# Performance work log

Measured on AMD Instinct MI355X. Metric: run time of the kernel, lower is better.

The kernel has to match this reference:

```python
import jax, jax.numpy as jnp
import numpy as np

N_PIX = 196608  # 12 * 128**2 (HEALPix nside=128)
F = 32          # filters (Fin == Fout for residual)
DM = 2          # depth multiplier


def _cheb_sep_conv(x, idx, wnb, wd, wp, b):
    """Separable Chebyshev graph conv.
    x: [B,N,F] maps; idx: [N,nb] neighbor indices; wnb: [N,nb] Laplacian weights;
    wd: [K,F,DM] depthwise Chebyshev weights; wp: [F*DM,Fout] pointwise; b: [Fout].
    """
    def L(t):  # sparse Laplacian apply via fixed-degree neighbor gather
        return jnp.einsum('bnjf,nj->bnf', t[:, idx, :], wnb)
    K = wd.shape[0]
    Ts = [x, L(x)]
    for _ in range(K - 2):  # Chebyshev recursion T_k = 2 L T_{k-1} - T_{k-2}
        Ts.append(2.0 * L(Ts[-1]) - Ts[-2])
    T = jnp.stack(Ts, 0)                      # [K,B,N,F]
    y = jnp.einsum('kbnf,kfd->bnfd', T, wd)   # depthwise over Chebyshev orders
    Bb, Nn, Ff, Dd = y.shape
    y = y.reshape(Bb, Nn, Ff * Dd)
    return y @ wp + b                         # pointwise mix to Fout


def _layernorm(x, gamma, beta, eps=1e-6):
    mu = jnp.mean(x, axis=-1, keepdims=True)
    var = jnp.mean(jnp.square(x - mu), axis=-1, keepdims=True)
    return (x - mu) * jax.lax.rsqrt(var + eps) * gamma + beta


def setup_inputs() -> dict:
    key = jax.random.key(0)
    ks = jax.random.split(key, 10)
    inp = {
        'maps': jax.random.normal(ks[0], (1, N_PIX, F), jnp.float32),
        'idx1': jax.random.randint(ks[1], (N_PIX, 8), 0, N_PIX, jnp.int32),
        'w1_nb': jax.random.normal(ks[2], (N_PIX, 8), jnp.float32) * 0.1,
        'idx2': jax.random.randint(ks[3], (N_PIX, 20), 0, N_PIX, jnp.int32),
        'w2_nb': jax.random.normal(ks[4], (N_PIX, 20), jnp.float32) * 0.1,
        'wd1': jax.random.normal(ks[5], (6, F, DM), jnp.float32) * 0.1,
        'wp1': jax.random.normal(ks[6], (F * DM, F), jnp.float32) * 0.1,
        'b1': jnp.zeros((F,), jnp.float32),
        'gamma1': jnp.ones((F,), jnp.float32),
        'beta1': jnp.zeros((F,), jnp.float32),
        'wd2': jax.random.normal(ks[7], (10, F, DM), jnp.float32) * 0.1,
        'wp2': jax.random.normal(ks[8], (F * DM, F), jnp.float32) * 0.1,
        'b2': jnp.zeros((F,), jnp.float32),
        'gamma2': jnp.ones((F,), jnp.float32),
        'beta2': jnp.zeros((F,), jnp.float32),
    }
    return inp


def reference(maps, idx1, w1_nb, idx2, w2_nb, wd1, wp1, b1, gamma1, beta1,
              wd2, wp2, b2, gamma2, beta2):
    res = maps
    x = _cheb_sep_conv(maps, idx1, w1_nb, wd1, wp1, b1)   # K=6, nb=8
    x = jax.nn.relu(x)
    x = _layernorm(x, gamma1, beta1)
    x = _cheb_sep_conv(x, idx2, w2_nb, wd2, wp2, b2)      # K=10, nb=20
    x = jax.nn.relu(x)
    x = _layernorm(x, gamma2, beta2)
    return x + res
```

## Files before the change

### kernel.cpp

```cpp
#include <hip/hip_runtime.h>

constexpr int NPIX = 196608;
constexpr int FF   = 32;
constexpr size_t SLOT = (size_t)NPIX * FF;

typedef short bf16x8 __attribute__((ext_vector_type(8)));
typedef float f32x4  __attribute__((ext_vector_type(4)));

__device__ __forceinline__ float blo(uint u) {
    union { float f; uint i; } v; v.i = u << 16; return v.f;
}
__device__ __forceinline__ float bhi(uint u) {
    union { float f; uint i; } v; v.i = u & 0xffff0000u; return v.f;
}
__device__ __forceinline__ ushort f2b(float f) {
    union { float f; uint i; } v; v.f = f;
    uint r = v.i + 0x7fffu + ((v.i >> 16) & 1u);
    return (ushort)(r >> 16);
}
__device__ __forceinline__ uint pack2(float lo, float hi) {
    return ((uint)f2b(hi) << 16) | (uint)f2b(lo);
}

__global__ __launch_bounds__(256) void f2b_kernel(const float* __restrict__ src,
                                                  ushort* __restrict__ dst) {
    int i = (blockIdx.x * 256 + threadIdx.x) * 4;
    float4 v = *reinterpret_cast<const float4*>(src + i);
    ushort4 o;
    o.x = f2b(v.x); o.y = f2b(v.y); o.z = f2b(v.z); o.w = f2b(v.w);
    *reinterpret_cast<ushort4*>(dst + i) = o;
}

template<int NB, bool INIT>
__global__ __launch_bounds__(256, 4) void cheb_step4(
    const ushort* __restrict__ Tprev,
    const ushort* __restrict__ Told,
    ushort*       __restrict__ Tout,
    const int*    __restrict__ idx,
    const float*  __restrict__ wnb)
{
    int t = blockIdx.x * 256 + threadIdx.x;
    int n = t >> 2;
    int h = t & 3;

    const int4*   ip = reinterpret_cast<const int4*>(idx + (size_t)n * NB);
    const float4* wv = reinterpret_cast<const float4*>(wnb + (size_t)n * NB);
    int4   I[NB / 4];
    float4 W[NB / 4];
#pragma unroll
    for (int j = 0; j < NB / 4; ++j) { I[j] = ip[j]; W[j] = wv[j]; }

    const uint4* Tp = reinterpret_cast<const uint4*>(Tprev);
    float s0 = 0.f, s1 = 0.f, s2 = 0.f, s3 = 0.f;
    float s4 = 0.f, s5 = 0.f, s6 = 0.f, s7 = 0.f;

#pragma unroll
    for (int j = 0; j < NB / 4; ++j) {
        int4 i4 = I[j]; float4 w4 = W[j];
        {
            uint4 u = Tp[(size_t)i4.x * 4 + h];
            s0 += w4.x * blo(u.x); s1 += w4.x * bhi(u.x);
            s2 += w4.x * blo(u.y); s3 += w4.x * bhi(u.y);
            s4 += w4.x * blo(u.z); s5 += w4.x * bhi(u.z);
            s6 += w4.x * blo(u.w); s7 += w4.x * bhi(u.w);
        }
        {
            uint4 u = Tp[(size_t)i4.y * 4 + h];
            s0 += w4.y * blo(u.x); s1 += w4.y * bhi(u.x);
            s2 += w4.y * blo(u.y); s3 += w4.y * bhi(u.y);
            s4 += w4.y * blo(u.z); s5 += w4.y * bhi(u.z);
            s6 += w4.y * blo(u.w); s7 += w4.y * bhi(u.w);
        }
        {
            uint4 u = Tp[(size_t)i4.z * 4 + h];
            s0 += w4.z * blo(u.x); s1 += w4.z * bhi(u.x);
            s2 += w4.z * blo(u.y); s3 += w4.z * bhi(u.y);
            s4 += w4.z * blo(u.z); s5 += w4.z * bhi(u.z);
            s6 += w4.z * blo(u.w); s7 += w4.z * bhi(u.w);
        }
        {
            uint4 u = Tp[(size_t)i4.w * 4 + h];
            s0 += w4.w * blo(u.x); s1 += w4.w * bhi(u.x);
            s2 += w4.w * blo(u.y); s3 += w4.w * bhi(u.y);
            s4 += w4.w * blo(u.z); s5 += w4.w * bhi(u.z);
            s6 += w4.w * blo(u.w); s7 += w4.w * bhi(u.w);
        }
    }

    size_t base = (size_t)n * 4 + h;
    uint4 o;
    if (INIT) {
        o.x = pack2(s0, s1); o.y = pack2(s2, s3);
        o.z = pack2(s4, s5); o.w = pack2(s6, s7);
    } else {
        uint4 told = reinterpret_cast<const uint4*>(Told)[base];
        o.x = pack2(2.f * s0 - blo(told.x), 2.f * s1 - bhi(told.x));
        o.y = pack2(2.f * s2 - blo(told.y), 2.f * s3 - bhi(told.y));
        o.z = pack2(2.f * s4 - blo(told.z), 2.f * s5 - bhi(told.z));
        o.w = pack2(2.f * s6 - blo(told.w), 2.f * s7 - bhi(told.w));
    }
    reinterpret_cast<uint4*>(Tout)[base] = o;
}

template<int K, bool RESIDUAL, bool OUT_BF16>
__global__ __launch_bounds__(256, 4) void finish_gemm(
    const ushort* __restrict__ chain,
    const float*  __restrict__ wd,
    const float*  __restrict__ wp,
    const float*  __restrict__ bias,
    const float*  __restrict__ gamma,
    const float*  __restrict__ beta,
    const float*  __restrict__ resid,
    void*         __restrict__ outp)
{
    constexpr int KW = K * 32;
    constexpr int WSTRIDE = KW + 8;
    __shared__ float swp[64 * 33];
    __shared__ __align__(16) ushort sW[32][WSTRIDE];

    int tid = threadIdx.x;
    int wv = tid >> 6, l = tid & 63;
    int r = l & 15, hi = l >> 4;
    int nbase = blockIdx.x * 64 + wv * 16;

    bf16x8 aF[K];
#pragma unroll
    for (int k = 0; k < K; ++k)
        aF[k] = *reinterpret_cast<const bf16x8*>(
            chain + (size_t)k * SLOT + (size_t)(nbase + r) * FF + hi * 8);

    for (int i = tid; i < 64 * 32; i += 256) {
        int u = i >> 5, g = i & 31;
        swp[u * 33 + g] = wp[i];
    }
    __syncthreads();

    for (int i = tid; i < 32 * KW; i += 256) {
        int g = i / KW, kf = i - g * KW;
        int f = kf & 31;
        float2 wdv = *reinterpret_cast<const float2*>(wd + (size_t)kf * 2);
        float w2 = wdv.x * swp[(2 * f) * 33 + g] + wdv.y * swp[(2 * f + 1) * 33 + g];
        sW[g][kf] = f2b(w2);
    }
    __syncthreads();

    f32x4 acc0 = {0.f, 0.f, 0.f, 0.f};
    f32x4 acc1 = {0.f, 0.f, 0.f, 0.f};
#pragma unroll
    for (int k = 0; k < K; ++k) {
        bf16x8 b0 = *reinterpret_cast<const bf16x8*>(&sW[r][k * 32 + hi * 8]);
        bf16x8 b1 = *reinterpret_cast<const bf16x8*>(&sW[16 + r][k * 32 + hi * 8]);
        acc0 = __builtin_amdgcn_mfma_f32_16x16x32_bf16(aF[k], b0, acc0, 0, 0, 0);
        acc1 = __builtin_amdgcn_mfma_f32_16x16x32_bf16(aF[k], b1, acc1, 0, 0, 0);
    }

    float bias_lo = bias[r],  bias_hi = bias[16 + r];
    float gam_lo  = gamma[r], gam_hi  = gamma[16 + r];
    float bet_lo  = beta[r],  bet_hi  = beta[16 + r];

#pragma unroll
    for (int v = 0; v < 4; ++v) {
        acc0[v] = fmaxf(acc0[v] + bias_lo, 0.f);
        acc1[v] = fmaxf(acc1[v] + bias_hi, 0.f);
    }
#pragma unroll
    for (int v = 0; v < 4; ++v) {
        float s1 = acc0[v] + acc1[v];
        float s2 = acc0[v] * acc0[v] + acc1[v] * acc1[v];
#pragma unroll
        for (int m = 1; m < 16; m <<= 1) {
            s1 += __shfl_xor(s1, m);
            s2 += __shfl_xor(s2, m);
        }
        float mu  = s1 * (1.f / 32.f);
        float var = s2 * (1.f / 32.f) - mu * mu;
        float rs  = rsqrtf(var + 1e-6f);
        int n = nbase + hi * 4 + v;
        size_t o0 = (size_t)n * FF + r;
        size_t o1 = o0 + 16;
        float z0 = (acc0[v] - mu) * rs * gam_lo + bet_lo;
        float z1 = (acc1[v] - mu) * rs * gam_hi + bet_hi;
        if (RESIDUAL) { z0 += resid[o0]; z1 += resid[o1]; }
        if (OUT_BF16) {
            ((ushort*)outp)[o0] = f2b(z0);
            ((ushort*)outp)[o1] = f2b(z1);
        } else {
            ((float*)outp)[o0] = z0;
            ((float*)outp)[o1] = z1;
        }
    }
}

extern "C" void kernel_launch(void* const* d_in, const int* in_sizes, int n_in,
                              void* d_out, int out_size, void* d_ws, size_t ws_size,
                              hipStream_t stream) {
    const float* maps = (const float*)d_in[0];
    const int*   idx1 = (const int*)  d_in[1];
    const float* w1nb = (const float*)d_in[2];
    const int*   idx2 = (const int*)  d_in[3];
    const float* w2nb = (const float*)d_in[4];
    const float* wd1  = (const float*)d_in[5];
    const float* wp1  = (const float*)d_in[6];
    const float* b1   = (const float*)d_in[7];
    const float* g1   = (const float*)d_in[8];
    const float* be1  = (const float*)d_in[9];
    const float* wd2  = (const float*)d_in[10];
    const float* wp2  = (const float*)d_in[11];
    const float* b2   = (const float*)d_in[12];
    const float* g2   = (const float*)d_in[13];
    const float* be2  = (const float*)d_in[14];
    float* out = (float*)d_out;

    ushort* slots = (ushort*)d_ws;
    ushort* B = slots;
    ushort* A = slots + 4 * SLOT;

    const int stepBlocks = NPIX * 4 / 256;
    const int cvtBlocks  = NPIX * FF / (256 * 4);
    const int finBlocks  = NPIX / 64;

    f2b_kernel<<<cvtBlocks, 256, 0, stream>>>(maps, A);
    cheb_step4<8, true><<<stepBlocks, 256, 0, stream>>>(A, nullptr, A + SLOT, idx1, w1nb);
    cheb_step4<8, false><<<stepBlocks, 256, 0, stream>>>(A + SLOT,     A,              A + 2 * SLOT, idx1, w1nb);
    cheb_step4<8, false><<<stepBlocks, 256, 0, stream>>>(A + 2 * SLOT, A + SLOT,       A + 3 * SLOT, idx1, w1nb);
    cheb_step4<8, false><<<stepBlocks, 256, 0, stream>>>(A + 3 * SLOT, A + 2 * SLOT,   A + 4 * SLOT, idx1, w1nb);
    cheb_step4<8, false><<<stepBlocks, 256, 0, stream>>>(A + 4 * SLOT, A + 3 * SLOT,   A + 5 * SLOT, idx1, w1nb);
    finish_gemm<6, false, true><<<finBlocks, 256, 0, stream>>>(A, wd1, wp1, b1, g1, be1, nullptr, B);

    cheb_step4<20, true><<<stepBlocks, 256, 0, stream>>>(B, nullptr, B + SLOT, idx2, w2nb);
    for (int k = 2; k <= 9; ++k)
        cheb_step4<20, false><<<stepBlocks, 256, 0, stream>>>(
            B + (size_t)(k - 1) * SLOT, B + (size_t)(k - 2) * SLOT,
            B + (size_t)k * SLOT, idx2, w2nb);
    finish_gemm<10, true, false><<<finBlocks, 256, 0, stream>>>(B, wd2, wp2, b2, g2, be2, maps, out);
}
```

Measured before the change: 766.2 us.

## Split feature maps into four planar 8-channel groups for cache-local gathers

After: 1.397 ms. 82.3% more time.

```diff
diff --git a/kernel.cpp b/kernel.cpp
--- a/kernel.cpp
+++ b/kernel.cpp
@@ -6,6 +6,8 @@
 
 typedef short bf16x8 __attribute__((ext_vector_type(8)));
 typedef float f32x4  __attribute__((ext_vector_type(4)));
+typedef int   i32x4  __attribute__((ext_vector_type(4)));
+typedef uint  u32x4  __attribute__((ext_vector_type(4)));
 
 __device__ __forceinline__ float blo(uint u) {
     union { float f; uint i; } v; v.i = u << 16; return v.f;
@@ -22,87 +24,76 @@
     return ((uint)f2b(hi) << 16) | (uint)f2b(lo);
 }
 
-__global__ __launch_bounds__(256) void f2b_kernel(const float* __restrict__ src,
-                                                  ushort* __restrict__ dst) {
-    int i = (blockIdx.x * 256 + threadIdx.x) * 4;
-    float4 v = *reinterpret_cast<const float4*>(src + i);
-    ushort4 o;
-    o.x = f2b(v.x); o.y = f2b(v.y); o.z = f2b(v.z); o.w = f2b(v.w);
-    *reinterpret_cast<ushort4*>(dst + i) = o;
+__global__ __launch_bounds__(256) void regroup_f2b(const float* __restrict__ src,
+                                                   ushort* __restrict__ dst) {
+    int t = blockIdx.x * 256 + threadIdx.x;
+    int n = t >> 2, g = t & 3;
+    const f32x4* sp = reinterpret_cast<const f32x4*>(src + (size_t)n * FF + g * 8);
+    f32x4 a = sp[0], b = sp[1];
+    u32x4 o;
+    o.x = pack2(a.x, a.y); o.y = pack2(a.z, a.w);
+    o.z = pack2(b.x, b.y); o.w = pack2(b.z, b.w);
+    reinterpret_cast<u32x4*>(dst)[(size_t)g * NPIX + n] = o;
 }
 
 template<int NB, bool INIT>
-__global__ __launch_bounds__(256, 4) void cheb_step4(
+__global__ __launch_bounds__(256, 4) void cheb_stepG(
     const ushort* __restrict__ Tprev,
     const ushort* __restrict__ Told,
     ushort*       __restrict__ Tout,
     const int*    __restrict__ idx,
     const float*  __restrict__ wnb)
 {
-    int t = blockIdx.x * 256 + threadIdx.x;
-    int n = t >> 2;
-    int h = t & 3;
-
-    const int4*   ip = reinterpret_cast<const int4*>(idx + (size_t)n * NB);
-    const float4* wv = reinterpret_cast<const float4*>(wnb + (size_t)n * NB);
-    int4   I[NB / 4];
-    float4 W[NB / 4];
-#pragma unroll
-    for (int j = 0; j < NB / 4; ++j) { I[j] = ip[j]; W[j] = wv[j]; }
-
-    const uint4* Tp = reinterpret_cast<const uint4*>(Tprev);
+    int b = blockIdx.x;
+    int g = b & 3;
+    int n = (b >> 2) * 256 + threadIdx.x;
+
+    i32x4 I[NB / 4];
+    f32x4 W[NB / 4];
+    const i32x4* ip = reinterpret_cast<const i32x4*>(idx + (size_t)n * NB);
+    const f32x4* wv = reinterpret_cast<const f32x4*>(wnb + (size_t)n * NB);
+#pragma unroll
+    for (int j = 0; j < NB / 4; ++j) {
+        I[j] = __builtin_nontemporal_load(ip + j);
+        W[j] = __builtin_nontemporal_load(wv + j);
+    }
+
+    const u32x4* Tp = reinterpret_cast<const u32x4*>(Tprev) + (size_t)g * NPIX;
     float s0 = 0.f, s1 = 0.f, s2 = 0.f, s3 = 0.f;
     float s4 = 0.f, s5 = 0.f, s6 = 0.f, s7 = 0.f;
 
 #pragma unroll
     for (int j = 0; j < NB / 4; ++j) {
-        int4 i4 = I[j]; float4 w4 = W[j];
-        {
-            uint4 u = Tp[(size_t)i4.x * 4 + h];
-            s0 += w4.x * blo(u.x); s1 += w4.x * bhi(u.x);
-            s2 += w4.x * blo(u.y); s3 += w4.x * bhi(u.y);
-            s4 += w4.x * blo(u.z); s5 += w4.x * bhi(u.z);
-            s6 += w4.x * blo(u.w); s7 += w4.x * bhi(u.w);
-        }
-        {
-            uint4 u = Tp[(size_t)i4.y * 4 + h];
-            s0 += w4.y * blo(u.x); s1 += w4.y * bhi(u.x);
-            s2 += w4.y * blo(u.y); s3 += w4.y * bhi(u.y);
-            s4 += w4.y * blo(u.z); s5 += w4.y * bhi(u.z);
-            s6 += w4.y * blo(u.w); s7 += w4.y * bhi(u.w);
-        }
-        {
-            uint4 u = Tp[(size_t)i4.z * 4 + h];
-            s0 += w4.z * blo(u.x); s1 += w4.z * bhi(u.x);
-            s2 += w4.z * blo(u.y); s3 += w4.z * bhi(u.y);
-            s4 += w4.z * blo(u.z); s5 += w4.z * bhi(u.z);
-            s6 += w4.z * blo(u.w); s7 += w4.z * bhi(u.w);
-        }
-        {
-            uint4 u = Tp[(size_t)i4.w * 4 + h];
-            s0 += w4.w * blo(u.x); s1 += w4.w * bhi(u.x);
-            s2 += w4.w * blo(u.y); s3 += w4.w * bhi(u.y);
-            s4 += w4.w * blo(u.z); s5 += w4.w * bhi(u.z);
-            s6 += w4.w * blo(u.w); s7 += w4.w * bhi(u.w);
-        }
-    }
-
-    size_t base = (size_t)n * 4 + h;
-    uint4 o;
+        i32x4 i4 = I[j]; f32x4 w4 = W[j];
+#pragma unroll
+        for (int e = 0; e < 4; ++e) {
+            int   ii = (e == 0) ? i4.x : (e == 1) ? i4.y : (e == 2) ? i4.z : i4.w;
+            float ww = (e == 0) ? w4.x : (e == 1) ? w4.y : (e == 2) ? w4.z : w4.w;
+            u32x4 u = Tp[(size_t)ii];
+            s0 += ww * blo(u.x); s1 += ww * bhi(u.x);
+            s2 += ww * blo(u.y); s3 += ww * bhi(u.y);
+            s4 += ww * blo(u.z); s5 += ww * bhi(u.z);
+            s6 += ww * blo(u.w); s7 += ww * bhi(u.w);
+        }
+    }
+
+    size_t row = (size_t)g * NPIX + n;
+    u32x4 o;
     if (INIT) {
         o.x = pack2(s0, s1); o.y = pack2(s2, s3);
         o.z = pack2(s4, s5); o.w = pack2(s6, s7);
     } else {
-        uint4 told = reinterpret_cast<const uint4*>(Told)[base];
+        u32x4 told = __builtin_nontemporal_load(
+            reinterpret_cast<const u32x4*>(Told) + row);
         o.x = pack2(2.f * s0 - blo(told.x), 2.f * s1 - bhi(told.x));
         o.y = pack2(2.f * s2 - blo(told.y), 2.f * s3 - bhi(told.y));
         o.z = pack2(2.f * s4 - blo(told.z), 2.f * s5 - bhi(told.z));
         o.w = pack2(2.f * s6 - blo(told.w), 2.f * s7 - bhi(told.w));
     }
-    reinterpret_cast<uint4*>(Tout)[base] = o;
-}
-
-template<int K, bool RESIDUAL, bool OUT_BF16>
+    __builtin_nontemporal_store(o, reinterpret_cast<u32x4*>(Tout) + row);
+}
+
+template<int K, bool RESIDUAL, bool OUT_GROUPED_BF16>
 __global__ __launch_bounds__(256, 4) void finish_gemm(
     const ushort* __restrict__ chain,
     const float*  __restrict__ wd,
@@ -127,20 +118,20 @@
 #pragma unroll
     for (int k = 0; k < K; ++k)
         aF[k] = *reinterpret_cast<const bf16x8*>(
-            chain + (size_t)k * SLOT + (size_t)(nbase + r) * FF + hi * 8);
+            chain + (size_t)k * SLOT + ((size_t)hi * NPIX + (nbase + r)) * 8);
 
     for (int i = tid; i < 64 * 32; i += 256) {
-        int u = i >> 5, g = i & 31;
-        swp[u * 33 + g] = wp[i];
+        int u = i >> 5, gg = i & 31;
+        swp[u * 33 + gg] = wp[i];
     }
     __syncthreads();
 
     for (int i = tid; i < 32 * KW; i += 256) {
-        int g = i / KW, kf = i - g * KW;
+        int gg = i / KW, kf = i - gg * KW;
         int f = kf & 31;
         float2 wdv = *reinterpret_cast<const float2*>(wd + (size_t)kf * 2);
-        float w2 = wdv.x * swp[(2 * f) * 33 + g] + wdv.y * swp[(2 * f + 1) * 33 + g];
-        sW[g][kf] = f2b(w2);
+        float w2 = wdv.x * swp[(2 * f) * 33 + gg] + wdv.y * swp[(2 * f + 1) * 33 + gg];
+        sW[gg][kf] = f2b(w2);
     }
     __syncthreads();
 
@@ -176,17 +167,21 @@
         float var = s2 * (1.f / 32.f) - mu * mu;
         float rs  = rsqrtf(var + 1e-6f);
         int n = nbase + hi * 4 + v;
-        size_t o0 = (size_t)n * FF + r;
-        size_t o1 = o0 + 16;
         float z0 = (acc0[v] - mu) * rs * gam_lo + bet_lo;
         float z1 = (acc1[v] - mu) * rs * gam_hi + bet_hi;
-        if (RESIDUAL) { z0 += resid[o0]; z1 += resid[o1]; }
-        if (OUT_BF16) {
-            ((ushort*)outp)[o0] = f2b(z0);
-            ((ushort*)outp)[o1] = f2b(z1);
+        if (RESIDUAL) {
+            z0 += resid[(size_t)n * FF + r];
+            z1 += resid[(size_t)n * FF + 16 + r];
+        }
+        if (OUT_GROUPED_BF16) {
+            ushort* op = (ushort*)outp;
+            int f0 = r, f1 = 16 + r;
+            op[((size_t)(f0 >> 3) * NPIX + n) * 8 + (f0 & 7)] = f2b(z0);
+            op[((size_t)(f1 >> 3) * NPIX + n) * 8 + (f1 & 7)] = f2b(z1);
         } else {
-            ((float*)outp)[o0] = z0;
-            ((float*)outp)[o1] = z1;
+            float* op = (float*)outp;
+            op[(size_t)n * FF + r]      = z0;
+            op[(size_t)n * FF + 16 + r] = z1;
         }
     }
 }
@@ -216,20 +211,19 @@
     ushort* A = slots + 4 * SLOT;
 
     const int stepBlocks = NPIX * 4 / 256;
-    const int cvtBlocks  = NPIX * FF / (256 * 4);
     const int finBlocks  = NPIX / 64;
 
-    f2b_kernel<<<cvtBlocks, 256, 0, stream>>>(maps, A);
-    cheb_step4<8, true><<<stepBlocks, 256, 0, stream>>>(A, nullptr, A + SLOT, idx1, w1nb);
-    cheb_step4<8, false><<<stepBlocks, 256, 0, stream>>>(A + SLOT,     A,              A + 2 * SLOT, idx1, w1nb);
-    cheb_step4<8, false><<<stepBlocks, 256, 0, stream>>>(A + 2 * SLOT, A + SLOT,       A + 3 * SLOT, idx1, w1nb);
-    cheb_step4<8, false><<<stepBlocks, 256, 0, stream>>>(A + 3 * SLOT, A + 2 * SLOT,   A + 4 * SLOT, idx1, w1nb);
-    cheb_step4<8, false><<<stepBlocks, 256, 0, stream>>>(A + 4 * SLOT, A + 3 * SLOT,   A + 5 * SLOT, idx1, w1nb);
+    regroup_f2b<<<stepBlocks, 256, 0, stream>>>(maps, A);
+    cheb_stepG<8, true><<<stepBlocks, 256, 0, stream>>>(A, nullptr, A + SLOT, idx1, w1nb);
+    cheb_stepG<8, false><<<stepBlocks, 256, 0, stream>>>(A + SLOT,     A,              A + 2 * SLOT, idx1, w1nb);
+    cheb_stepG<8, false><<<stepBlocks, 256, 0, stream>>>(A + 2 * SLOT, A + SLOT,       A + 3 * SLOT, idx1, w1nb);
+    cheb_stepG<8, false><<<stepBlocks, 256, 0, stream>>>(A + 3 * SLOT, A + 2 * SLOT,   A + 4 * SLOT, idx1, w1nb);
+    cheb_stepG<8, false><<<stepBlocks, 256, 0, stream>>>(A + 4 * SLOT, A + 3 * SLOT,   A + 5 * SLOT, idx1, w1nb);
     finish_gemm<6, false, true><<<finBlocks, 256, 0, stream>>>(A, wd1, wp1, b1, g1, be1, nullptr, B);
 
-    cheb_step4<20, true><<<stepBlocks, 256, 0, stream>>>(B, nullptr, B + SLOT, idx2, w2nb);
+    cheb_stepG<20, true><<<stepBlocks, 256, 0, stream>>>(B, nullptr, B + SLOT, idx2, w2nb);
     for (int k = 2; k <= 9; ++k)
-        cheb_step4<20, false><<<stepBlocks, 256, 0, stream>>>(
+        cheb_stepG<20, false><<<stepBlocks, 256, 0, stream>>>(
             B + (size_t)(k - 1) * SLOT, B + (size_t)(k - 2) * SLOT,
             B + (size_t)k * SLOT, idx2, w2nb);
     finish_gemm<10, true, false><<<finBlocks, 256, 0, stream>>>(B, wd2, wp2, b2, g2, be2, maps, out);
```
